# Optimization experiments

Measured on AMD Instinct MI355X. Metric: run time of the kernel, lower is better.

## Reference

```python
import jax, jax.numpy as jnp
import numpy as np

N_LEVELS = 9

def _avg_pool_2x2(x):
    # tf.nn.avg_pool2d(ksize=2, strides=2, padding='SAME'); H,W even at every
    # level for H=W=512, so SAME == VALID == simple 2x2 mean.
    b, h, w, c = x.shape
    return x.reshape(b, h // 2, 2, w // 2, 2, c).mean(axis=(2, 4))

def setup_inputs() -> dict:
    key = jax.random.key(0)
    x = jax.random.normal(key, (8, 512, 512, 2), dtype=jnp.float32)
    return {"x": x}

def reference(x):
    B, H, W, C = x.shape
    levels = [x]
    cur = x
    for _ in range(N_LEVELS - 1):
        cur = _avg_pool_2x2(cur)
        levels.append(cur)
    # tf.image.resize bilinear (half-pixel centers, no antialias on upsample)
    # == jax.image.resize method='bilinear' for upscaling.
    ups = [jax.image.resize(lv, (B, H, W, C), method='bilinear') for lv in levels]
    stacked = jnp.concatenate(ups, axis=-1)          # [B, H, W, 9*C]
    stacked = stacked[:, None]                       # [B, 1, H, W, 9*C]
    return jnp.transpose(stacked, (0, 4, 2, 3, 1))   # [B, 9*C, H, W, 1]
```

## Files before the change

### kernel.cpp

```cpp
#include <hip/hip_runtime.h>


#define HWTOT (512 * 512)

template <int S>
__global__ __launch_bounds__(256) void pool2x2(const float* __restrict__ src,
                                               float* __restrict__ dst) {
  int idx = blockIdx.x * blockDim.x + threadIdx.x;
  if (idx >= 8 * S * S) return;
  int j = idx & (S - 1);
  int t = idx / S;
  int i = t & (S - 1);
  int b = t / S;
  const int Sin = 2 * S;
  size_t base0 = ((size_t)(b * Sin + 2 * i) * Sin + 2 * j) * 2;
  size_t base1 = base0 + (size_t)Sin * 2;
  float4 a = *(const float4*)(src + base0);
  float4 c = *(const float4*)(src + base1);
  float2 o;
  o.x = (a.x + a.z + c.x + c.z) * 0.25f;
  o.y = (a.y + a.w + c.y + c.w) * 0.25f;
  *(float2*)(dst + (size_t)idx * 2) = o;
}

__global__ __launch_bounds__(256) void upsample_all(const float* __restrict__ x,
                                                    const float2* __restrict__ pyr,
                                                    float* __restrict__ out) {
  const int w = blockIdx.x * blockDim.x + threadIdx.x;
  const int h = blockIdx.y;
  const int b = blockIdx.z;

  const size_t obase = (size_t)b * 18 * HWTOT + (size_t)h * 512 + w;

  float2 v0 = ((const float2*)x)[((size_t)b * 512 + h) * 512 + w];
  out[obase] = v0.x;
  out[obase + HWTOT] = v0.y;

  const int off2[9] = {0, 0, 524288, 655360, 688128, 696320, 698368, 698880, 699008};

#pragma unroll
  for (int lv = 1; lv <= 8; ++lv) {
    const int S = 512 >> lv;
    const float scale = 1.0f / (float)(1 << lv);
    float sh = ((float)h + 0.5f) * scale - 0.5f;
    float sw = ((float)w + 0.5f) * scale - 0.5f;
    float fh0 = floorf(sh), fw0 = floorf(sw);
    float fh = sh - fh0, fw = sw - fw0;
    int h0 = (int)fh0, w0 = (int)fw0;
    int h0c = h0 < 0 ? 0 : h0;
    int h1c = (h0 + 1 > S - 1) ? (S - 1) : (h0 + 1);
    int w0c = w0 < 0 ? 0 : w0;
    int w1c = (w0 + 1 > S - 1) ? (S - 1) : (w0 + 1);

    const float2* L = pyr + off2[lv];
    size_t r0 = (size_t)(b * S + h0c) * S;
    size_t r1 = (size_t)(b * S + h1c) * S;
    float2 v00 = L[r0 + w0c];
    float2 v01 = L[r0 + w1c];
    float2 v10 = L[r1 + w0c];
    float2 v11 = L[r1 + w1c];

    float wx0 = 1.0f - fw, wy0 = 1.0f - fh;
    float tx = v00.x * wx0 + v01.x * fw;
    float ty = v00.y * wx0 + v01.y * fw;
    float bx = v10.x * wx0 + v11.x * fw;
    float by = v10.y * wx0 + v11.y * fw;
    float rx = tx * wy0 + bx * fh;
    float ry = ty * wy0 + by * fh;

    out[obase + (size_t)(2 * lv) * HWTOT] = rx;
    out[obase + (size_t)(2 * lv + 1) * HWTOT] = ry;
  }
}

extern "C" void kernel_launch(void* const* d_in, const int* in_sizes, int n_in,
                              void* d_out, int out_size, void* d_ws, size_t ws_size,
                              hipStream_t stream) {
  const float* x = (const float*)d_in[0];
  float* out = (float*)d_out;
  float* pyr = (float*)d_ws;

  const int offf[9] = {0, 0, 1048576, 1310720, 1376256, 1392640, 1396736, 1397760, 1398016};

  pool2x2<256><<<dim3((8 * 256 * 256 + 255) / 256), 256, 0, stream>>>(x, pyr + offf[1]);
  pool2x2<128><<<dim3((8 * 128 * 128 + 255) / 256), 256, 0, stream>>>(pyr + offf[1], pyr + offf[2]);
  pool2x2<64><<<dim3((8 * 64 * 64 + 255) / 256), 256, 0, stream>>>(pyr + offf[2], pyr + offf[3]);
  pool2x2<32><<<dim3((8 * 32 * 32 + 255) / 256), 256, 0, stream>>>(pyr + offf[3], pyr + offf[4]);
  pool2x2<16><<<dim3((8 * 16 * 16 + 255) / 256), 256, 0, stream>>>(pyr + offf[4], pyr + offf[5]);
  pool2x2<8><<<dim3((8 * 8 * 8 + 255) / 256), 256, 0, stream>>>(pyr + offf[5], pyr + offf[6]);
  pool2x2<4><<<dim3((8 * 4 * 4 + 255) / 256), 256, 0, stream>>>(pyr + offf[6], pyr + offf[7]);
  pool2x2<2><<<dim3((8 * 2 * 2 + 255) / 256), 256, 0, stream>>>(pyr + offf[7], pyr + offf[8]);

  upsample_all<<<dim3(512 / 256, 512, 8), 256, 0, stream>>>(x, (const float2*)pyr, out);
}
```

Measured before the change: 189.7 us.

## Fuse pyramid levels via shared memory and vectorize upsample with nontemporal stores

Replaces eight separate pool launches with one tiled kernel that builds levels 1-6 in shared memory per 64x64 tile, plus a tiny kernel for levels 7-8. This removes launch overhead and intermediate global round-trips. The upsample kernel now handles four adjacent pixels per thread and writes float4 nontemporal stores, cutting store instruction count and cache pollution for the large output. The small level-6/7/8 kernels still serialize, and the per-thread register use grows.

```diff
diff --git a/kernel.cpp b/kernel.cpp
--- a/kernel.cpp
+++ b/kernel.cpp
@@ -3,38 +3,123 @@
 
 #define HWTOT (512 * 512)
 
-template <int S>
-__global__ __launch_bounds__(256) void pool2x2(const float* __restrict__ src,
-                                               float* __restrict__ dst) {
-  int idx = blockIdx.x * blockDim.x + threadIdx.x;
-  if (idx >= 8 * S * S) return;
-  int j = idx & (S - 1);
-  int t = idx / S;
-  int i = t & (S - 1);
-  int b = t / S;
-  const int Sin = 2 * S;
-  size_t base0 = ((size_t)(b * Sin + 2 * i) * Sin + 2 * j) * 2;
-  size_t base1 = base0 + (size_t)Sin * 2;
-  float4 a = *(const float4*)(src + base0);
-  float4 c = *(const float4*)(src + base1);
-  float2 o;
-  o.x = (a.x + a.z + c.x + c.z) * 0.25f;
-  o.y = (a.y + a.w + c.y + c.w) * 0.25f;
-  *(float2*)(dst + (size_t)idx * 2) = o;
+typedef float vfloat4 __attribute__((ext_vector_type(4)));
+
+__global__ __launch_bounds__(256) void build_levels_1_6(const float* __restrict__ x,
+                                                        float2* __restrict__ pyr) {
+  const int b = blockIdx.y;
+  const int tx = blockIdx.x & 7, ty = blockIdx.x >> 3;
+  const int t = threadIdx.x;
+
+  __shared__ float2 sh1[32 * 32];
+  __shared__ float2 sh2[16 * 16];
+  __shared__ float2 sh3[8 * 8];
+  __shared__ float2 sh4[4 * 4];
+  __shared__ float2 sh5[2 * 2];
+
+  {
+    const int i = t >> 3;
+    const int j0 = (t & 7) << 2;
+    const float* r0 = x + (((size_t)(b * 512 + ty * 64 + 2 * i)) * 512 + (tx * 64 + 2 * j0)) * 2;
+    const float* r1 = r0 + 1024;
+    float2 o[4];
+#pragma unroll
+    for (int k = 0; k < 4; ++k) {
+      float4 a = *(const float4*)(r0 + 4 * k);
+      float4 c = *(const float4*)(r1 + 4 * k);
+      o[k].x = (a.x + a.z + c.x + c.z) * 0.25f;
+      o[k].y = (a.y + a.w + c.y + c.w) * 0.25f;
+      sh1[i * 32 + j0 + k] = o[k];
+    }
+    float2* g = pyr + ((size_t)(b * 256 + ty * 32 + i) * 256 + tx * 32 + j0);
+    *(float4*)(g) = make_float4(o[0].x, o[0].y, o[1].x, o[1].y);
+    *(float4*)(g + 2) = make_float4(o[2].x, o[2].y, o[3].x, o[3].y);
+  }
+  __syncthreads();
+  {
+    const int i = t >> 4, j = t & 15;
+    float2 a = sh1[(2 * i) * 32 + 2 * j], c = sh1[(2 * i) * 32 + 2 * j + 1];
+    float2 d = sh1[(2 * i + 1) * 32 + 2 * j], e = sh1[(2 * i + 1) * 32 + 2 * j + 1];
+    float2 o = {(a.x + c.x + d.x + e.x) * 0.25f, (a.y + c.y + d.y + e.y) * 0.25f};
+    sh2[i * 16 + j] = o;
+    pyr[524288 + (size_t)(b * 128 + ty * 16 + i) * 128 + tx * 16 + j] = o;
+  }
+  __syncthreads();
+  if (t < 64) {
+    const int i = t >> 3, j = t & 7;
+    float2 a = sh2[(2 * i) * 16 + 2 * j], c = sh2[(2 * i) * 16 + 2 * j + 1];
+    float2 d = sh2[(2 * i + 1) * 16 + 2 * j], e = sh2[(2 * i + 1) * 16 + 2 * j + 1];
+    float2 o = {(a.x + c.x + d.x + e.x) * 0.25f, (a.y + c.y + d.y + e.y) * 0.25f};
+    sh3[i * 8 + j] = o;
+    pyr[655360 + (size_t)(b * 64 + ty * 8 + i) * 64 + tx * 8 + j] = o;
+  }
+  __syncthreads();
+  if (t < 16) {
+    const int i = t >> 2, j = t & 3;
+    float2 a = sh3[(2 * i) * 8 + 2 * j], c = sh3[(2 * i) * 8 + 2 * j + 1];
+    float2 d = sh3[(2 * i + 1) * 8 + 2 * j], e = sh3[(2 * i + 1) * 8 + 2 * j + 1];
+    float2 o = {(a.x + c.x + d.x + e.x) * 0.25f, (a.y + c.y + d.y + e.y) * 0.25f};
+    sh4[i * 4 + j] = o;
+    pyr[688128 + (size_t)(b * 32 + ty * 4 + i) * 32 + tx * 4 + j] = o;
+  }
+  __syncthreads();
+  if (t < 4) {
+    const int i = t >> 1, j = t & 1;
+    float2 a = sh4[(2 * i) * 4 + 2 * j], c = sh4[(2 * i) * 4 + 2 * j + 1];
+    float2 d = sh4[(2 * i + 1) * 4 + 2 * j], e = sh4[(2 * i + 1) * 4 + 2 * j + 1];
+    float2 o = {(a.x + c.x + d.x + e.x) * 0.25f, (a.y + c.y + d.y + e.y) * 0.25f};
+    sh5[i * 2 + j] = o;
+    pyr[696320 + (size_t)(b * 16 + ty * 2 + i) * 16 + tx * 2 + j] = o;
+  }
+  __syncthreads();
+  if (t == 0) {
+    float2 a = sh5[0], c = sh5[1], d = sh5[2], e = sh5[3];
+    float2 o = {(a.x + c.x + d.x + e.x) * 0.25f, (a.y + c.y + d.y + e.y) * 0.25f};
+    pyr[698368 + (size_t)(b * 8 + ty) * 8 + tx] = o;
+  }
+}
+
+__global__ __launch_bounds__(64) void build_levels_7_8(float2* __restrict__ pyr) {
+  const int b = blockIdx.x;
+  const int t = threadIdx.x;
+  __shared__ float2 s7[16];
+  const float2* l6 = pyr + 698368 + (size_t)b * 64;
+  if (t < 16) {
+    const int i = t >> 2, j = t & 3;
+    float2 a = l6[(2 * i) * 8 + 2 * j], c = l6[(2 * i) * 8 + 2 * j + 1];
+    float2 d = l6[(2 * i + 1) * 8 + 2 * j], e = l6[(2 * i + 1) * 8 + 2 * j + 1];
+    float2 o = {(a.x + c.x + d.x + e.x) * 0.25f, (a.y + c.y + d.y + e.y) * 0.25f};
+    s7[t] = o;
+    pyr[698880 + (size_t)b * 16 + t] = o;
+  }
+  __syncthreads();
+  if (t < 4) {
+    const int i = t >> 1, j = t & 1;
+    float2 a = s7[(2 * i) * 4 + 2 * j], c = s7[(2 * i) * 4 + 2 * j + 1];
+    float2 d = s7[(2 * i + 1) * 4 + 2 * j], e = s7[(2 * i + 1) * 4 + 2 * j + 1];
+    float2 o = {(a.x + c.x + d.x + e.x) * 0.25f, (a.y + c.y + d.y + e.y) * 0.25f};
+    pyr[699008 + (size_t)b * 4 + t] = o;
+  }
 }
 
 __global__ __launch_bounds__(256) void upsample_all(const float* __restrict__ x,
                                                     const float2* __restrict__ pyr,
                                                     float* __restrict__ out) {
-  const int w = blockIdx.x * blockDim.x + threadIdx.x;
-  const int h = blockIdx.y;
-  const int b = blockIdx.z;
+  const int t = threadIdx.x;
+  const int w0pix = (t & 127) << 2;
+  const int h = (blockIdx.x << 1) + (t >> 7);
+  const int b = blockIdx.y;
+  const size_t obase = (size_t)b * 18 * HWTOT + (size_t)h * 512 + w0pix;
 
-  const size_t obase = (size_t)b * 18 * HWTOT + (size_t)h * 512 + w;
-
-  float2 v0 = ((const float2*)x)[((size_t)b * 512 + h) * 512 + w];
-  out[obase] = v0.x;
-  out[obase + HWTOT] = v0.y;
+  {
+    const float* px = x + (((size_t)b * 512 + h) * 512 + w0pix) * 2;
+    float4 a = *(const float4*)px;
+    float4 c = *(const float4*)(px + 4);
+    vfloat4 ch0 = {a.x, a.z, c.x, c.z};
+    vfloat4 ch1 = {a.y, a.w, c.y, c.w};
+    __builtin_nontemporal_store(ch0, (vfloat4*)(out + obase));
+    __builtin_nontemporal_store(ch1, (vfloat4*)(out + obase + HWTOT));
+  }
 
   const int off2[9] = {0, 0, 524288, 655360, 688128, 696320, 698368, 698880, 699008};
 
@@ -43,33 +128,38 @@
     const int S = 512 >> lv;
     const float scale = 1.0f / (float)(1 << lv);
     float sh = ((float)h + 0.5f) * scale - 0.5f;
-    float sw = ((float)w + 0.5f) * scale - 0.5f;
-    float fh0 = floorf(sh), fw0 = floorf(sw);
-    float fh = sh - fh0, fw = sw - fw0;
-    int h0 = (int)fh0, w0 = (int)fw0;
+    float fh0f = floorf(sh);
+    float fh = sh - fh0f;
+    int h0 = (int)fh0f;
     int h0c = h0 < 0 ? 0 : h0;
     int h1c = (h0 + 1 > S - 1) ? (S - 1) : (h0 + 1);
-    int w0c = w0 < 0 ? 0 : w0;
-    int w1c = (w0 + 1 > S - 1) ? (S - 1) : (w0 + 1);
+    const float2* R0 = pyr + off2[lv] + (size_t)(b * S + h0c) * S;
+    const float2* R1 = pyr + off2[lv] + (size_t)(b * S + h1c) * S;
+    const float wy0 = 1.0f - fh;
 
-    const float2* L = pyr + off2[lv];
-    size_t r0 = (size_t)(b * S + h0c) * S;
-    size_t r1 = (size_t)(b * S + h1c) * S;
-    float2 v00 = L[r0 + w0c];
-    float2 v01 = L[r0 + w1c];
-    float2 v10 = L[r1 + w0c];
-    float2 v11 = L[r1 + w1c];
-
-    float wx0 = 1.0f - fw, wy0 = 1.0f - fh;
-    float tx = v00.x * wx0 + v01.x * fw;
-    float ty = v00.y * wx0 + v01.y * fw;
-    float bx = v10.x * wx0 + v11.x * fw;
-    float by = v10.y * wx0 + v11.y * fw;
-    float rx = tx * wy0 + bx * fh;
-    float ry = ty * wy0 + by * fh;
-
-    out[obase + (size_t)(2 * lv) * HWTOT] = rx;
-    out[obase + (size_t)(2 * lv + 1) * HWTOT] = ry;
+    float o0[4], o1[4];
+#pragma unroll
+    for (int k = 0; k < 4; ++k) {
+      float sw = ((float)(w0pix + k) + 0.5f) * scale - 0.5f;
+      float fw0f = floorf(sw);
+      float fw = sw - fw0f;
+      int w0 = (int)fw0f;
+      int w0c = w0 < 0 ? 0 : w0;
+      int w1c = (w0 + 1 > S - 1) ? (S - 1) : (w0 + 1);
+      float2 v00 = R0[w0c], v01 = R0[w1c];
+      float2 v10 = R1[w0c], v11 = R1[w1c];
+      float wx0 = 1.0f - fw;
+      float tx_ = v00.x * wx0 + v01.x * fw;
+      float bx_ = v10.x * wx0 + v11.x * fw;
+      float ty_ = v00.y * wx0 + v01.y * fw;
+      float by_ = v10.y * wx0 + v11.y * fw;
+      o0[k] = tx_ * wy0 + bx_ * fh;
+      o1[k] = ty_ * wy0 + by_ * fh;
+    }
+    vfloat4 c0 = {o0[0], o0[1], o0[2], o0[3]};
+    vfloat4 c1 = {o1[0], o1[1], o1[2], o1[3]};
+    __builtin_nontemporal_store(c0, (vfloat4*)(out + obase + (size_t)(2 * lv) * HWTOT));
+    __builtin_nontemporal_store(c1, (vfloat4*)(out + obase + (size_t)(2 * lv + 1) * HWTOT));
   }
 }
 
@@ -78,18 +168,9 @@
                               hipStream_t stream) {
   const float* x = (const float*)d_in[0];
   float* out = (float*)d_out;
-  float* pyr = (float*)d_ws;
+  float2* pyr = (float2*)d_ws;
 
-  const int offf[9] = {0, 0, 1048576, 1310720, 1376256, 1392640, 1396736, 1397760, 1398016};
-
-  pool2x2<256><<<dim3((8 * 256 * 256 + 255) / 256), 256, 0, stream>>>(x, pyr + offf[1]);
-  pool2x2<128><<<dim3((8 * 128 * 128 + 255) / 256), 256, 0, stream>>>(pyr + offf[1], pyr + offf[2]);
-  pool2x2<64><<<dim3((8 * 64 * 64 + 255) / 256), 256, 0, stream>>>(pyr + offf[2], pyr + offf[3]);
-  pool2x2<32><<<dim3((8 * 32 * 32 + 255) / 256), 256, 0, stream>>>(pyr + offf[3], pyr + offf[4]);
-  pool2x2<16><<<dim3((8 * 16 * 16 + 255) / 256), 256, 0, stream>>>(pyr + offf[4], pyr + offf[5]);
-  pool2x2<8><<<dim3((8 * 8 * 8 + 255) / 256), 256, 0, stream>>>(pyr + offf[5], pyr + offf[6]);
-  pool2x2<4><<<dim3((8 * 4 * 4 + 255) / 256), 256, 0, stream>>>(pyr + offf[6], pyr + offf[7]);
-  pool2x2<2><<<dim3((8 * 2 * 2 + 255) / 256), 256, 0, stream>>>(pyr + offf[7], pyr + offf[8]);
-
-  upsample_all<<<dim3(512 / 256, 512, 8), 256, 0, stream>>>(x, (const float2*)pyr, out);
+  build_levels_1_6<<<dim3(64, 8), 256, 0, stream>>>(x, pyr);
+  build_levels_7_8<<<dim3(8), 64, 0, stream>>>(pyr);
+  upsample_all<<<dim3(256, 8), 256, 0, stream>>>(x, pyr, out);
 }
```

New measurement: 178.9 us. 1.06x faster.
